# Performance work log

Measured on AMD Instinct MI355X. Metric: run time of the kernel, lower is better.

The kernel has to match this reference:

```python
import jax, jax.numpy as jnp
import numpy as np

E, T, D_H, D_I, R = 8, 4096, 2048, 5632, 128


def setup_inputs() -> dict:
    key = jax.random.key(0)
    ks = jax.random.split(key, 12)
    s = 0.02
    return {
        "x": jax.random.normal(ks[0], (T, D_H), dtype=jnp.float32),
        "expert_idx": jax.random.randint(ks[1], (T,), 0, E),
        # gate: hidden -> intermediate
        "gate_A": jax.random.normal(ks[2], (E, R, D_H), dtype=jnp.float32) * s,
        "gate_C": jax.random.normal(ks[3], (R, R), dtype=jnp.float32) * s,
        "gate_B": jax.random.normal(ks[4], (E, D_I, R), dtype=jnp.float32) * s,
        # up: hidden -> intermediate
        "up_A": jax.random.normal(ks[5], (E, R, D_H), dtype=jnp.float32) * s,
        "up_C": jax.random.normal(ks[6], (R, R), dtype=jnp.float32) * s,
        "up_B": jax.random.normal(ks[7], (E, D_I, R), dtype=jnp.float32) * s,
        # down: intermediate -> hidden, with per-expert bias
        "down_A": jax.random.normal(ks[8], (E, R, D_I), dtype=jnp.float32) * s,
        "down_C": jax.random.normal(ks[9], (R, R), dtype=jnp.float32) * s,
        "down_B": jax.random.normal(ks[10], (E, D_H, R), dtype=jnp.float32) * s,
        "down_bias": jax.random.normal(ks[11], (E, D_H), dtype=jnp.float32) * s,
    }


def _shared_core(x, A, C, B, onehot_et):
    # x: [t, d_in]; A: [e, r, d_in]; C: [r, r]; B: [e, d_out, r]; onehot_et: [e, t]
    # per-token expert weight W_e = B_e @ C @ A_e; mask early so zeros propagate
    h = jnp.einsum('td,erd->etr', x, A) * onehot_et[:, :, None]  # [e, t, r]
    h = jnp.einsum('etr,sr->ets', h, C)                           # [e, t, r]
    return jnp.einsum('ets,eds->td', h, B)                        # [t, d_out]


def reference(x, expert_idx, gate_A, gate_C, gate_B, up_A, up_C, up_B,
              down_A, down_C, down_B, down_bias):
    onehot = jax.nn.one_hot(expert_idx, E, dtype=x.dtype).T  # [E, T]
    g = jax.nn.silu(_shared_core(x, gate_A, gate_C, gate_B, onehot))  # [T, D_I]
    u = _shared_core(x, up_A, up_C, up_B, onehot)                     # [T, D_I]
    down = _shared_core(g * u, down_A, down_C, down_B, onehot)        # [T, D_H]
    return down + down_bias[expert_idx]
```

## Files before the change

### kernel.cpp

```cpp
#include <hip/hip_runtime.h>
#include <hip/hip_bf16.h>

#define E_  8
#define T_  4096
#define DH_ 2048
#define DI_ 5632
#define R_  128
#define TILE_ 64
#define NT_ 72
#define TPMAX_ (NT_*TILE_)

typedef short bf16x8 __attribute__((ext_vector_type(8)));
typedef short bf16x4 __attribute__((ext_vector_type(4)));
typedef float f32x4 __attribute__((ext_vector_type(4)));

#define MFMA(a, b, c) __builtin_amdgcn_mfma_f32_16x16x32_bf16((a), (b), (c), 0, 0, 0)

__device__ __forceinline__ unsigned short f2bf(float f) {
  union { float f; unsigned u; } v; v.f = f;
  return (unsigned short)((v.u + 0x7fffu + ((v.u >> 16) & 1u)) >> 16);
}

__device__ __forceinline__ bf16x8 cvt8(float4 a, float4 b) {
  bf16x8 o;
  o[0] = (short)f2bf(a.x); o[1] = (short)f2bf(a.y);
  o[2] = (short)f2bf(a.z); o[3] = (short)f2bf(a.w);
  o[4] = (short)f2bf(b.x); o[5] = (short)f2bf(b.y);
  o[6] = (short)f2bf(b.z); o[7] = (short)f2bf(b.w);
  return o;
}

__device__ __forceinline__ int tile_expert(int s0, const int* off) {
  int e = 0;
#pragma unroll
  for (int q = 1; q < E_; q++) if (s0 >= off[q]) e = q;
  return e;
}

__global__ __launch_bounds__(1024) void k_route(
    const int* __restrict__ idx, int* __restrict__ off, int* __restrict__ tok)
{
  __shared__ int cnt[E_], cur[E_], offs[E_ + 1];
  const int tid = threadIdx.x;
  if (tid < E_) cnt[tid] = 0;
  __syncthreads();
  for (int t = tid; t < T_; t += 1024) atomicAdd(&cnt[idx[t]], 1);
  __syncthreads();
  if (tid == 0) {
    int a = 0;
    for (int e = 0; e < E_; e++) {
      offs[e] = a; cur[e] = a;
      a += ((cnt[e] + TILE_ - 1) / TILE_) * TILE_;
    }
    offs[E_] = a;
  }
  __syncthreads();
  if (tid <= E_) off[tid] = offs[tid];
  for (int t = tid; t < T_; t += 1024) {
    int p = atomicAdd(&cur[idx[t]], 1);
    tok[p] = t;
  }
}

__global__ __launch_bounds__(256) void k_cvt(
    const float* __restrict__ gA, const float* __restrict__ uA,
    const float* __restrict__ gB, const float* __restrict__ uB,
    const float* __restrict__ dA, const float* __restrict__ dB,
    const float* __restrict__ gC, const float* __restrict__ uC,
    const float* __restrict__ dC,
    short* __restrict__ gAb, short* __restrict__ uAb,
    short* __restrict__ gBb, short* __restrict__ uBb,
    short* __restrict__ dAb, short* __restrict__ dBb,
    short* __restrict__ gCb, short* __restrict__ uCb,
    short* __restrict__ dCb)
{
  long i = (long)(blockIdx.x * 256 + threadIdx.x) * 4;
  const float* s; short* d;
  if      (i <  4194304) { if (i < 2097152) { s = gA; d = gAb; } else { s = uA; d = uAb; i -= 2097152; } }
  else if (i <  9961472) { s = gB; d = gBb; i -= 4194304; }
  else if (i < 15728640) { s = uB; d = uBb; i -= 9961472; }
  else if (i < 21495808) { s = dA; d = dAb; i -= 15728640; }
  else if (i < 23592960) { s = dB; d = dBb; i -= 21495808; }
  else if (i < 23609344) { s = gC; d = gCb; i -= 23592960; }
  else if (i < 23625728) { s = uC; d = uCb; i -= 23609344; }
  else if (i < 23642112) { s = dC; d = dCb; i -= 23625728; }
  else return;
  float4 v = *(const float4*)(s + i);
  bf16x4 o;
  o[0] = (short)f2bf(v.x); o[1] = (short)f2bf(v.y);
  o[2] = (short)f2bf(v.z); o[3] = (short)f2bf(v.w);
  *(bf16x4*)(d + i) = o;
}

__global__ __launch_bounds__(256) void k_gather(
    const float* __restrict__ x, const int* __restrict__ tok,
    short* __restrict__ Xb)
{
  const int p = blockIdx.x;
  const int t = tok[p];
  const int c = threadIdx.x * 8;
  bf16x8 o;
  if (t >= 0) {
    float4 v0 = *(const float4*)(x + (size_t)t * DH_ + c);
    float4 v1 = *(const float4*)(x + (size_t)t * DH_ + c + 4);
    o = cvt8(v0, v1);
  } else {
    o = (bf16x8){0, 0, 0, 0, 0, 0, 0, 0};
  }
  *(bf16x8*)(Xb + (size_t)p * DH_ + c) = o;
}

__global__ __launch_bounds__(256) void k_stage1(
    const short* __restrict__ Xb,
    const short* __restrict__ gAb, const short* __restrict__ uAb,
    const int* __restrict__ off, float* __restrict__ Hp)
{
  const int s0 = blockIdx.x * TILE_;
  if (s0 >= off[E_]) return;
  const int e = tile_expert(s0, off);
  const int y = blockIdx.y, kc = blockIdx.z;
  const short* A = (y ? uAb : gAb) + (size_t)e * R_ * DH_ + kc * 512;

  const int tid = threadIdx.x;
  const int lane = tid & 63, wv = tid >> 6;
  const int col = lane & 15, quad = lane >> 4;

  const short* xb = Xb + (size_t)(s0 + col) * DH_ + kc * 512 + quad * 8;
  const short* ab = A + (size_t)(wv * 32 + col) * DH_ + quad * 8;

  f32x4 acc[4][2] = {};
#pragma unroll 4
  for (int k0 = 0; k0 < 512; k0 += 32) {
    bf16x8 b0 = *(const bf16x8*)(ab + k0);
    bf16x8 b1 = *(const bf16x8*)(ab + (size_t)16 * DH_ + k0);
#pragma unroll
    for (int m = 0; m < 4; m++) {
      bf16x8 a = *(const bf16x8*)(xb + (size_t)m * 16 * DH_ + k0);
      acc[m][0] = MFMA(a, b0, acc[m][0]);
      acc[m][1] = MFMA(a, b1, acc[m][1]);
    }
  }
  float* O = Hp + (size_t)(y * 4 + kc) * TPMAX_ * R_;
#pragma unroll
  for (int m = 0; m < 4; m++)
#pragma unroll
    for (int nl = 0; nl < 2; nl++)
#pragma unroll
      for (int r = 0; r < 4; r++)
        O[(size_t)(s0 + m * 16 + quad * 4 + r) * R_ + (wv * 2 + nl) * 16 + col] =
            acc[m][nl][r];
}

__global__ __launch_bounds__(256) void k_stage1b(
    const float* __restrict__ Hp,
    const short* __restrict__ gCb, const short* __restrict__ uCb,
    const int* __restrict__ off,
    short* __restrict__ Hgb, short* __restrict__ Hub)
{
  const int s0 = blockIdx.x * TILE_;
  if (s0 >= off[E_]) return;
  const int y = blockIdx.y;
  const short* C = y ? uCb : gCb;
  short* H = y ? Hub : Hgb;

  __shared__ short h1s[64][136];
  const int tid = threadIdx.x;
  {
    const int lg = tid >> 2, lq = (tid & 3) * 32;
    const float* base = Hp + ((size_t)y * 4 * TPMAX_ + s0 + lg) * R_ + lq;
    float s[32] = {};
#pragma unroll
    for (int kc = 0; kc < 4; kc++) {
      const float* p = base + (size_t)kc * TPMAX_ * R_;
#pragma unroll
      for (int q = 0; q < 8; q++) {
        float4 v = *(const float4*)(p + q * 4);
        s[q * 4 + 0] += v.x; s[q * 4 + 1] += v.y;
        s[q * 4 + 2] += v.z; s[q * 4 + 3] += v.w;
      }
    }
#pragma unroll
    for (int j = 0; j < 32; j++) h1s[lg][lq + j] = (short)f2bf(s[j]);
  }
  __syncthreads();

  const int lane = tid & 63, wv = tid >> 6;
  const int col = lane & 15, quad = lane >> 4;
  f32x4 acc2[4][2] = {};
#pragma unroll
  for (int kk = 0; kk < 4; kk++) {
    bf16x8 b[2];
#pragma unroll
    for (int nl = 0; nl < 2; nl++)
      b[nl] = *(const bf16x8*)(C + (size_t)((wv * 2 + nl) * 16 + col) * R_ +
                               kk * 32 + quad * 8);
#pragma unroll
    for (int m = 0; m < 4; m++) {
      bf16x8 a = *(const bf16x8*)&h1s[m * 16 + col][kk * 32 + quad * 8];
      acc2[m][0] = MFMA(a, b[0], acc2[m][0]);
      acc2[m][1] = MFMA(a, b[1], acc2[m][1]);
    }
  }
#pragma unroll
  for (int m = 0; m < 4; m++)
#pragma unroll
    for (int nl = 0; nl < 2; nl++)
#pragma unroll
      for (int r = 0; r < 4; r++)
        H[(size_t)(s0 + m * 16 + quad * 4 + r) * R_ + (wv * 2 + nl) * 16 + col] =
            (short)f2bf(acc2[m][nl][r]);
}

__global__ __launch_bounds__(256, 2) void k_stage2(
    const short* __restrict__ Hgb, const short* __restrict__ Hub,
    const short* __restrict__ gBb, const short* __restrict__ uBb,
    const short* __restrict__ dAb,
    const int* __restrict__ off, float* __restrict__ Hd1)
{
  const int e = blockIdx.x;
  const int i0 = blockIdx.y * 128;
  const int lo = off[e], hi = off[e + 1];
  if (lo >= hi) return;
  const short* Bg = gBb + (size_t)e * DI_ * R_;
  const short* Bu = uBb + (size_t)e * DI_ * R_;
  const short* Ad = dAb + (size_t)e * R_ * DI_;

  const int tid = threadIdx.x;
  const int lane = tid & 63, wv = tid >> 6;
  const int col = lane & 15, quad = lane >> 4;

  bf16x8 wg[4][2], wu[4][2], wa[4][2];
#pragma unroll
  for (int kk = 0; kk < 4; kk++)
#pragma unroll
    for (int nl = 0; nl < 2; nl++) {
      size_t bo = (size_t)(i0 + (wv * 2 + nl) * 16 + col) * R_ + kk * 32 + quad * 8;
      wg[kk][nl] = *(const bf16x8*)(Bg + bo);
      wu[kk][nl] = *(const bf16x8*)(Bu + bo);
      wa[kk][nl] = *(const bf16x8*)(Ad + (size_t)((wv * 2 + nl) * 16 + col) * DI_ +
                                    i0 + kk * 32 + quad * 8);
    }

  __shared__ short hgs[64][136];
  __shared__ short hus[64][136];
  __shared__ short ZT[64][136];

  for (int s0 = lo; s0 < hi; s0 += TILE_) {
    {
      const int row = tid >> 2, seg = (tid & 3) * 32;
      const short* pg = Hgb + (size_t)(s0 + row) * R_ + seg;
      const short* pu = Hub + (size_t)(s0 + row) * R_ + seg;
#pragma unroll
      for (int q = 0; q < 4; q++) {
        *(bf16x8*)&hgs[row][seg + q * 8] = *(const bf16x8*)(pg + q * 8);
        *(bf16x8*)&hus[row][seg + q * 8] = *(const bf16x8*)(pu + q * 8);
      }
    }
    __syncthreads();

    f32x4 gacc[4][2] = {}, uacc[4][2] = {};
#pragma unroll
    for (int kk = 0; kk < 4; kk++)
#pragma unroll
      for (int m = 0; m < 4; m++) {
        bf16x8 ag = *(const bf16x8*)&hgs[m * 16 + col][kk * 32 + quad * 8];
        bf16x8 au = *(const bf16x8*)&hus[m * 16 + col][kk * 32 + quad * 8];
#pragma unroll
        for (int nl = 0; nl < 2; nl++) {
          gacc[m][nl] = MFMA(ag, wg[kk][nl], gacc[m][nl]);
          uacc[m][nl] = MFMA(au, wu[kk][nl], uacc[m][nl]);
        }
      }
    __syncthreads();

#pragma unroll
    for (int m = 0; m < 4; m++)
#pragma unroll
      for (int nl = 0; nl < 2; nl++)
#pragma unroll
        for (int r = 0; r < 4; r++) {
          float g = gacc[m][nl][r];
          float z = (g / (1.0f + __expf(-g))) * uacc[m][nl][r];
          ZT[m * 16 + quad * 4 + r][(wv * 2 + nl) * 16 + col] = (short)f2bf(z);
        }
    __syncthreads();

    f32x4 dacc[4][2] = {};
#pragma unroll
    for (int kk2 = 0; kk2 < 4; kk2++)
#pragma unroll
      for (int m = 0; m < 4; m++) {
        bf16x8 za = *(const bf16x8*)&ZT[m * 16 + col][kk2 * 32 + quad * 8];
        dacc[m][0] = MFMA(za, wa[kk2][0], dacc[m][0]);
        dacc[m][1] = MFMA(za, wa[kk2][1], dacc[m][1]);
      }
#pragma unroll
    for (int m = 0; m < 4; m++)
#pragma unroll
      for (int nl = 0; nl < 2; nl++)
#pragma unroll
        for (int r = 0; r < 4; r++)
          atomicAdd(&Hd1[(size_t)(s0 + m * 16 + quad * 4 + r) * R_ +
                         (wv * 2 + nl) * 16 + col],
                    dacc[m][nl][r]);
  }
}

__global__ __launch_bounds__(256) void k_applyCd(
    const float* __restrict__ Hd1, const short* __restrict__ dCb,
    const int* __restrict__ off, short* __restrict__ Hd2b)
{
  const int s0 = blockIdx.x * TILE_;
  if (s0 >= off[E_]) return;
  const int tid = threadIdx.x;
  const int lane = tid & 63, wv = tid >> 6;
  const int col = lane & 15, quad = lane >> 4;

  bf16x8 wc[4][2];
#pragma unroll
  for (int kk = 0; kk < 4; kk++)
#pragma unroll
    for (int nl = 0; nl < 2; nl++)
      wc[kk][nl] = *(const bf16x8*)(dCb + (size_t)((wv * 2 + nl) * 16 + col) * R_ +
                                    kk * 32 + quad * 8);

  f32x4 acc[4][2] = {};
#pragma unroll
  for (int kk = 0; kk < 4; kk++)
#pragma unroll
    for (int m = 0; m < 4; m++) {
      const float* hp = Hd1 + (size_t)(s0 + m * 16 + col) * R_ + kk * 32 + quad * 8;
      float4 v0 = *(const float4*)hp;
      float4 v1 = *(const float4*)(hp + 4);
      bf16x8 a = cvt8(v0, v1);
      acc[m][0] = MFMA(a, wc[kk][0], acc[m][0]);
      acc[m][1] = MFMA(a, wc[kk][1], acc[m][1]);
    }
#pragma unroll
  for (int m = 0; m < 4; m++)
#pragma unroll
    for (int nl = 0; nl < 2; nl++)
#pragma unroll
      for (int r = 0; r < 4; r++)
        Hd2b[(size_t)(s0 + m * 16 + quad * 4 + r) * R_ + (wv * 2 + nl) * 16 + col] =
            (short)f2bf(acc[m][nl][r]);
}

__global__ __launch_bounds__(256, 2) void k_stage3(
    const short* __restrict__ Hd2b, const short* __restrict__ dBb,
    const float* __restrict__ dbias,
    const int* __restrict__ off, const int* __restrict__ tok,
    float* __restrict__ out)
{
  const int e = blockIdx.x;
  const int d0 = blockIdx.y * 128;
  const int lo = off[e], hi = off[e + 1];
  const int tid = threadIdx.x;
  const int lane = tid & 63, wv = tid >> 6;
  const int col = lane & 15, quad = lane >> 4;

  bf16x8 wb[4][2];
#pragma unroll
  for (int kk = 0; kk < 4; kk++)
#pragma unroll
    for (int nl = 0; nl < 2; nl++)
      wb[kk][nl] = *(const bf16x8*)(dBb + (size_t)e * DH_ * R_ +
                                    (size_t)(d0 + (wv * 2 + nl) * 16 + col) * R_ +
                                    kk * 32 + quad * 8);
  float bias[2];
#pragma unroll
  for (int nl = 0; nl < 2; nl++)
    bias[nl] = dbias[(size_t)e * DH_ + d0 + (wv * 2 + nl) * 16 + col];

  for (int s0 = lo + (int)blockIdx.z * TILE_; s0 < hi; s0 += 4 * TILE_) {
    f32x4 acc[4][2] = {};
#pragma unroll
    for (int kk = 0; kk < 4; kk++)
#pragma unroll
      for (int m = 0; m < 4; m++) {
        bf16x8 a = *(const bf16x8*)(Hd2b + (size_t)(s0 + m * 16 + col) * R_ +
                                    kk * 32 + quad * 8);
        acc[m][0] = MFMA(a, wb[kk][0], acc[m][0]);
        acc[m][1] = MFMA(a, wb[kk][1], acc[m][1]);
      }
#pragma unroll
    for (int m = 0; m < 4; m++)
#pragma unroll
      for (int r = 0; r < 4; r++) {
        int t = tok[s0 + m * 16 + quad * 4 + r];
        if (t < 0) continue;
#pragma unroll
        for (int nl = 0; nl < 2; nl++) {
          int d = d0 + (wv * 2 + nl) * 16 + col;
          out[(size_t)t * DH_ + d] = acc[m][nl][r] + bias[nl];
        }
      }
  }
}

extern "C" void kernel_launch(void* const* d_in, const int* in_sizes, int n_in,
                              void* d_out, int out_size, void* d_ws, size_t ws_size,
                              hipStream_t stream)
{
  (void)in_sizes; (void)n_in; (void)out_size; (void)ws_size;
  const float* x     = (const float*)d_in[0];
  const int*   idx   = (const int*)d_in[1];
  const float* gA    = (const float*)d_in[2];
  const float* gC    = (const float*)d_in[3];
  const float* gBw   = (const float*)d_in[4];
  const float* uA    = (const float*)d_in[5];
  const float* uC    = (const float*)d_in[6];
  const float* uBw   = (const float*)d_in[7];
  const float* dA    = (const float*)d_in[8];
  const float* dC    = (const float*)d_in[9];
  const float* dBw   = (const float*)d_in[10];
  const float* dbias = (const float*)d_in[11];
  float* out = (float*)d_out;

  char* ws = (char*)d_ws;
  int* off = (int*)ws;
  int* tok = (int*)(ws + 512);
  float* Hd1 = (float*)(ws + 32768);
  float* Hp  = (float*)(ws + 2392064);
  short* Xb  = (short*)(ws + 21266432);
  short* Hgb = (short*)(ws + 40140800);
  short* Hub = (short*)(ws + 41320448);
  short* Hd2b= (short*)(ws + 42500096);
  short* gAb = (short*)(ws + 43679744);
  short* uAb = (short*)(ws + 47874048);
  short* gBb = (short*)(ws + 52068352);
  short* uBb = (short*)(ws + 63602688);
  short* dAb = (short*)(ws + 75137024);
  short* dBb = (short*)(ws + 86671360);
  short* gCb = (short*)(ws + 90865664);
  short* uCb = (short*)(ws + 90898432);
  short* dCb = (short*)(ws + 90931200);

  hipMemsetAsync(tok, 0xFF, TPMAX_ * sizeof(int), stream);
  hipMemsetAsync(Hd1, 0, (size_t)TPMAX_ * R_ * sizeof(float), stream);

  k_cvt    <<<dim3(23088), 256, 0, stream>>>(gA, uA, gBw, uBw, dA, dBw, gC, uC, dC,
                                             gAb, uAb, gBb, uBb, dAb, dBb, gCb, uCb, dCb);
  k_route  <<<1, 1024, 0, stream>>>(idx, off, tok);
  k_gather <<<dim3(TPMAX_), 256, 0, stream>>>(x, tok, Xb);
  k_stage1 <<<dim3(NT_, 2, 4), 256, 0, stream>>>(Xb, gAb, uAb, off, Hp);
  k_stage1b<<<dim3(NT_, 2), 256, 0, stream>>>(Hp, gCb, uCb, off, Hgb, Hub);
  k_stage2 <<<dim3(E_, 44), 256, 0, stream>>>(Hgb, Hub, gBb, uBb, dAb, off, Hd1);
  k_applyCd<<<dim3(NT_), 256, 0, stream>>>(Hd1, dCb, off, Hd2b);
  k_stage3 <<<dim3(E_, 16, 4), 256, 0, stream>>>(Hd2b, dBb, dbias, off, tok, out);
}
```

Baseline: 349.7 us.

## Restructure MoE pipeline: fuse cvt+gather, drop split-K stage1, retile stage2 by token tile

Merges weight conversion and token gather into one launch. Stage1 now splits the output over the rank dimension instead of splitting K, so each block writes bf16 directly with no fp32 partial buffer and no reduction in stage1b. Stage2 moves from per-expert blocks that loop over all of that expert's tokens to per-token-tile blocks that each cover an eighth of the intermediate dimension, streaming the weights. Stage3 is launched with twice the z-parallelism. The changes trade weight reuse within a block for more parallelism and less intermediate memory traffic, and may reread weights more often from cache.

Measured after the change: 349.9 us. No clear change (+0.1%).

```diff
diff --git a/kernel.cpp b/kernel.cpp
--- a/kernel.cpp
+++ b/kernel.cpp
@@ -62,7 +62,9 @@
   }
 }
 
-__global__ __launch_bounds__(256) void k_cvt(
+__global__ __launch_bounds__(256) void k_cvtgather(
+    const float* __restrict__ x, const int* __restrict__ tok,
+    short* __restrict__ Xb,
     const float* __restrict__ gA, const float* __restrict__ uA,
     const float* __restrict__ gB, const float* __restrict__ uB,
     const float* __restrict__ dA, const float* __restrict__ dB,
@@ -74,7 +76,22 @@
     short* __restrict__ gCb, short* __restrict__ uCb,
     short* __restrict__ dCb)
 {
-  long i = (long)(blockIdx.x * 256 + threadIdx.x) * 4;
+  if (blockIdx.x < TPMAX_) {
+    const int p = blockIdx.x;
+    const int t = tok[p];
+    const int c = threadIdx.x * 8;
+    bf16x8 o;
+    if (t >= 0) {
+      float4 v0 = *(const float4*)(x + (size_t)t * DH_ + c);
+      float4 v1 = *(const float4*)(x + (size_t)t * DH_ + c + 4);
+      o = cvt8(v0, v1);
+    } else {
+      o = (bf16x8){0, 0, 0, 0, 0, 0, 0, 0};
+    }
+    *(bf16x8*)(Xb + (size_t)p * DH_ + c) = o;
+    return;
+  }
+  long i = (long)((blockIdx.x - TPMAX_) * 256 + threadIdx.x) * 4;
   const float* s; short* d;
   if      (i <  4194304) { if (i < 2097152) { s = gA; d = gAb; } else { s = uA; d = uAb; i -= 2097152; } }
   else if (i <  9961472) { s = gB; d = gBb; i -= 4194304; }
@@ -92,67 +109,53 @@
   *(bf16x4*)(d + i) = o;
 }
 
-__global__ __launch_bounds__(256) void k_gather(
-    const float* __restrict__ x, const int* __restrict__ tok,
-    short* __restrict__ Xb)
-{
-  const int p = blockIdx.x;
-  const int t = tok[p];
-  const int c = threadIdx.x * 8;
-  bf16x8 o;
-  if (t >= 0) {
-    float4 v0 = *(const float4*)(x + (size_t)t * DH_ + c);
-    float4 v1 = *(const float4*)(x + (size_t)t * DH_ + c + 4);
-    o = cvt8(v0, v1);
-  } else {
-    o = (bf16x8){0, 0, 0, 0, 0, 0, 0, 0};
-  }
-  *(bf16x8*)(Xb + (size_t)p * DH_ + c) = o;
-}
-
-__global__ __launch_bounds__(256) void k_stage1(
+__global__ __launch_bounds__(256, 2) void k_stage1(
     const short* __restrict__ Xb,
     const short* __restrict__ gAb, const short* __restrict__ uAb,
-    const int* __restrict__ off, float* __restrict__ Hp)
-{
-  const int s0 = blockIdx.x * TILE_;
+    const int* __restrict__ off,
+    short* __restrict__ h1gb, short* __restrict__ h1ub)
+{
+  const int id = blockIdx.x;
+  const int rh = id & 1, y = (id >> 1) & 1, tp = (id >> 2) & 1;
+  const int tl = (id >> 3) * 2 + tp;
+  const int s0 = tl * TILE_;
   if (s0 >= off[E_]) return;
   const int e = tile_expert(s0, off);
-  const int y = blockIdx.y, kc = blockIdx.z;
-  const short* A = (y ? uAb : gAb) + (size_t)e * R_ * DH_ + kc * 512;
+  const short* A = (y ? uAb : gAb) + (size_t)e * R_ * DH_ + (size_t)(rh * 64) * DH_;
+  short* H1 = y ? h1ub : h1gb;
 
   const int tid = threadIdx.x;
   const int lane = tid & 63, wv = tid >> 6;
   const int col = lane & 15, quad = lane >> 4;
 
-  const short* xb = Xb + (size_t)(s0 + col) * DH_ + kc * 512 + quad * 8;
-  const short* ab = A + (size_t)(wv * 32 + col) * DH_ + quad * 8;
-
-  f32x4 acc[4][2] = {};
-#pragma unroll 4
-  for (int k0 = 0; k0 < 512; k0 += 32) {
+  const short* xb = Xb + (size_t)(s0 + col) * DH_ + quad * 8;
+  const short* ab = A + (size_t)(wv * 16 + col) * DH_ + quad * 8;
+
+  f32x4 acc[4] = {};
+  for (int k0 = 0; k0 < DH_; k0 += 64) {
     bf16x8 b0 = *(const bf16x8*)(ab + k0);
-    bf16x8 b1 = *(const bf16x8*)(ab + (size_t)16 * DH_ + k0);
+    bf16x8 b1 = *(const bf16x8*)(ab + k0 + 32);
+    bf16x8 a0[4], a1[4];
 #pragma unroll
     for (int m = 0; m < 4; m++) {
-      bf16x8 a = *(const bf16x8*)(xb + (size_t)m * 16 * DH_ + k0);
-      acc[m][0] = MFMA(a, b0, acc[m][0]);
-      acc[m][1] = MFMA(a, b1, acc[m][1]);
-    }
-  }
-  float* O = Hp + (size_t)(y * 4 + kc) * TPMAX_ * R_;
+      a0[m] = *(const bf16x8*)(xb + (size_t)m * 16 * DH_ + k0);
+      a1[m] = *(const bf16x8*)(xb + (size_t)m * 16 * DH_ + k0 + 32);
+    }
+#pragma unroll
+    for (int m = 0; m < 4; m++) acc[m] = MFMA(a0[m], b0, acc[m]);
+#pragma unroll
+    for (int m = 0; m < 4; m++) acc[m] = MFMA(a1[m], b1, acc[m]);
+  }
 #pragma unroll
   for (int m = 0; m < 4; m++)
 #pragma unroll
-    for (int nl = 0; nl < 2; nl++)
-#pragma unroll
-      for (int r = 0; r < 4; r++)
-        O[(size_t)(s0 + m * 16 + quad * 4 + r) * R_ + (wv * 2 + nl) * 16 + col] =
-            acc[m][nl][r];
-}
-
-__global__ __launch_bounds__(256) void k_stage1b(
-    const float* __restrict__ Hp,
+    for (int r = 0; r < 4; r++)
+      H1[(size_t)(s0 + m * 16 + quad * 4 + r) * R_ + rh * 64 + wv * 16 + col] =
+          (short)f2bf(acc[m][r]);
+}
+
+__global__ __launch_bounds__(256, 2) void k_stage1b(
+    const short* __restrict__ h1gb, const short* __restrict__ h1ub,
     const short* __restrict__ gCb, const short* __restrict__ uCb,
     const int* __restrict__ off,
     short* __restrict__ Hgb, short* __restrict__ Hub)
@@ -160,27 +163,18 @@
   const int s0 = blockIdx.x * TILE_;
   if (s0 >= off[E_]) return;
   const int y = blockIdx.y;
+  const short* h1 = y ? h1ub : h1gb;
   const short* C = y ? uCb : gCb;
   short* H = y ? Hub : Hgb;
 
   __shared__ short h1s[64][136];
   const int tid = threadIdx.x;
   {
-    const int lg = tid >> 2, lq = (tid & 3) * 32;
-    const float* base = Hp + ((size_t)y * 4 * TPMAX_ + s0 + lg) * R_ + lq;
-    float s[32] = {};
-#pragma unroll
-    for (int kc = 0; kc < 4; kc++) {
-      const float* p = base + (size_t)kc * TPMAX_ * R_;
-#pragma unroll
-      for (int q = 0; q < 8; q++) {
-        float4 v = *(const float4*)(p + q * 4);
-        s[q * 4 + 0] += v.x; s[q * 4 + 1] += v.y;
-        s[q * 4 + 2] += v.z; s[q * 4 + 3] += v.w;
-      }
-    }
-#pragma unroll
-    for (int j = 0; j < 32; j++) h1s[lg][lq + j] = (short)f2bf(s[j]);
+    const int row = tid >> 2, seg = (tid & 3) * 32;
+    const short* p = h1 + (size_t)(s0 + row) * R_ + seg;
+#pragma unroll
+    for (int q = 0; q < 4; q++)
+      *(bf16x8*)&h1s[row][seg + q * 8] = *(const bf16x8*)(p + q * 8);
   }
   __syncthreads();
 
@@ -211,99 +205,95 @@
             (short)f2bf(acc2[m][nl][r]);
 }
 
-__global__ __launch_bounds__(256, 2) void k_stage2(
+__global__ __launch_bounds__(256, 3) void k_stage2(
     const short* __restrict__ Hgb, const short* __restrict__ Hub,
     const short* __restrict__ gBb, const short* __restrict__ uBb,
     const short* __restrict__ dAb,
     const int* __restrict__ off, float* __restrict__ Hd1)
 {
-  const int e = blockIdx.x;
-  const int i0 = blockIdx.y * 128;
-  const int lo = off[e], hi = off[e + 1];
-  if (lo >= hi) return;
+  const int id = blockIdx.x;
+  const int c = id & 7, tl = id >> 3;
+  const int s0 = tl * TILE_;
+  if (s0 >= off[E_]) return;
+  const int e = tile_expert(s0, off);
+  const int i0 = c * 704;
   const short* Bg = gBb + (size_t)e * DI_ * R_;
   const short* Bu = uBb + (size_t)e * DI_ * R_;
   const short* Ad = dAb + (size_t)e * R_ * DI_;
 
+  __shared__ short hgs[64][136];
+  __shared__ short hus[64][136];
+  __shared__ short ZT[64][72];
+
   const int tid = threadIdx.x;
   const int lane = tid & 63, wv = tid >> 6;
   const int col = lane & 15, quad = lane >> 4;
 
-  bf16x8 wg[4][2], wu[4][2], wa[4][2];
-#pragma unroll
-  for (int kk = 0; kk < 4; kk++)
-#pragma unroll
-    for (int nl = 0; nl < 2; nl++) {
-      size_t bo = (size_t)(i0 + (wv * 2 + nl) * 16 + col) * R_ + kk * 32 + quad * 8;
-      wg[kk][nl] = *(const bf16x8*)(Bg + bo);
-      wu[kk][nl] = *(const bf16x8*)(Bu + bo);
-      wa[kk][nl] = *(const bf16x8*)(Ad + (size_t)((wv * 2 + nl) * 16 + col) * DI_ +
-                                    i0 + kk * 32 + quad * 8);
-    }
-
-  __shared__ short hgs[64][136];
-  __shared__ short hus[64][136];
-  __shared__ short ZT[64][136];
-
-  for (int s0 = lo; s0 < hi; s0 += TILE_) {
-    {
-      const int row = tid >> 2, seg = (tid & 3) * 32;
-      const short* pg = Hgb + (size_t)(s0 + row) * R_ + seg;
-      const short* pu = Hub + (size_t)(s0 + row) * R_ + seg;
-#pragma unroll
-      for (int q = 0; q < 4; q++) {
-        *(bf16x8*)&hgs[row][seg + q * 8] = *(const bf16x8*)(pg + q * 8);
-        *(bf16x8*)&hus[row][seg + q * 8] = *(const bf16x8*)(pu + q * 8);
-      }
-    }
-    __syncthreads();
-
-    f32x4 gacc[4][2] = {}, uacc[4][2] = {};
-#pragma unroll
-    for (int kk = 0; kk < 4; kk++)
+  {
+    const int row = tid >> 2, seg = (tid & 3) * 32;
+    const short* pg = Hgb + (size_t)(s0 + row) * R_ + seg;
+    const short* pu = Hub + (size_t)(s0 + row) * R_ + seg;
+#pragma unroll
+    for (int q = 0; q < 4; q++) {
+      *(bf16x8*)&hgs[row][seg + q * 8] = *(const bf16x8*)(pg + q * 8);
+      *(bf16x8*)&hus[row][seg + q * 8] = *(const bf16x8*)(pu + q * 8);
+    }
+  }
+  __syncthreads();
+
+  f32x4 dacc[4][2] = {};
+
+  for (int sub = 0; sub < 11; sub++) {
+    const int ib = i0 + sub * 64;
+    const int cg = ib + wv * 16 + col;
+    f32x4 gacc[4] = {}, uacc[4] = {};
+#pragma unroll
+    for (int kk = 0; kk < 4; kk++) {
+      bf16x8 bg = *(const bf16x8*)(Bg + (size_t)cg * R_ + kk * 32 + quad * 8);
+      bf16x8 bu = *(const bf16x8*)(Bu + (size_t)cg * R_ + kk * 32 + quad * 8);
 #pragma unroll
       for (int m = 0; m < 4; m++) {
         bf16x8 ag = *(const bf16x8*)&hgs[m * 16 + col][kk * 32 + quad * 8];
         bf16x8 au = *(const bf16x8*)&hus[m * 16 + col][kk * 32 + quad * 8];
-#pragma unroll
-        for (int nl = 0; nl < 2; nl++) {
-          gacc[m][nl] = MFMA(ag, wg[kk][nl], gacc[m][nl]);
-          uacc[m][nl] = MFMA(au, wu[kk][nl], uacc[m][nl]);
-        }
+        gacc[m] = MFMA(ag, bg, gacc[m]);
+        uacc[m] = MFMA(au, bu, uacc[m]);
+      }
+    }
+    __syncthreads();
+#pragma unroll
+    for (int m = 0; m < 4; m++)
+#pragma unroll
+      for (int r = 0; r < 4; r++) {
+        float g = gacc[m][r];
+        float z = (g / (1.0f + __expf(-g))) * uacc[m][r];
+        ZT[m * 16 + quad * 4 + r][wv * 16 + col] = (short)f2bf(z);
       }
     __syncthreads();
-
-#pragma unroll
-    for (int m = 0; m < 4; m++)
-#pragma unroll
-      for (int nl = 0; nl < 2; nl++)
-#pragma unroll
-        for (int r = 0; r < 4; r++) {
-          float g = gacc[m][nl][r];
-          float z = (g / (1.0f + __expf(-g))) * uacc[m][nl][r];
-          ZT[m * 16 + quad * 4 + r][(wv * 2 + nl) * 16 + col] = (short)f2bf(z);
-        }
-    __syncthreads();
-
-    f32x4 dacc[4][2] = {};
-#pragma unroll
-    for (int kk2 = 0; kk2 < 4; kk2++)
-#pragma unroll
-      for (int m = 0; m < 4; m++) {
-        bf16x8 za = *(const bf16x8*)&ZT[m * 16 + col][kk2 * 32 + quad * 8];
-        dacc[m][0] = MFMA(za, wa[kk2][0], dacc[m][0]);
-        dacc[m][1] = MFMA(za, wa[kk2][1], dacc[m][1]);
+#pragma unroll
+    for (int kk2 = 0; kk2 < 2; kk2++) {
+      bf16x8 za[4];
+#pragma unroll
+      for (int m = 0; m < 4; m++)
+        za[m] = *(const bf16x8*)&ZT[m * 16 + col][kk2 * 32 + quad * 8];
+#pragma unroll
+      for (int nl = 0; nl < 2; nl++) {
+        bf16x8 ba = *(const bf16x8*)(Ad + (size_t)((wv * 2 + nl) * 16 + col) * DI_ +
+                                     ib + kk2 * 32 + quad * 8);
+#pragma unroll
+        for (int m = 0; m < 4; m++)
+          dacc[m][nl] = MFMA(za[m], ba, dacc[m][nl]);
       }
-#pragma unroll
-    for (int m = 0; m < 4; m++)
-#pragma unroll
-      for (int nl = 0; nl < 2; nl++)
-#pragma unroll
-        for (int r = 0; r < 4; r++)
-          atomicAdd(&Hd1[(size_t)(s0 + m * 16 + quad * 4 + r) * R_ +
-                         (wv * 2 + nl) * 16 + col],
-                    dacc[m][nl][r]);
-  }
+    }
+  }
+#pragma unroll
+  for (int m = 0; m < 4; m++)
+#pragma unroll
+    for (int nl = 0; nl < 2; nl++)
+#pragma unroll
+      for (int r = 0; r < 4; r++)
+        atomicAdd(&Hd1[(size_t)(s0 + m * 16 + quad * 4 + r) * R_ +
+                       (wv * 2 + nl) * 16 + col],
+                  dacc[m][nl][r]);
 }
 
 __global__ __launch_bounds__(256) void k_applyCd(
@@ -372,7 +362,7 @@
   for (int nl = 0; nl < 2; nl++)
     bias[nl] = dbias[(size_t)e * DH_ + d0 + (wv * 2 + nl) * 16 + col];
 
-  for (int s0 = lo + (int)blockIdx.z * TILE_; s0 < hi; s0 += 4 * TILE_) {
+  for (int s0 = lo + (int)blockIdx.z * TILE_; s0 < hi; s0 += 8 * TILE_) {
     f32x4 acc[4][2] = {};
 #pragma unroll
     for (int kk = 0; kk < 4; kk++)
@@ -421,31 +411,32 @@
   int* off = (int*)ws;
   int* tok = (int*)(ws + 512);
   float* Hd1 = (float*)(ws + 32768);
-  float* Hp  = (float*)(ws + 2392064);
-  short* Xb  = (short*)(ws + 21266432);
-  short* Hgb = (short*)(ws + 40140800);
-  short* Hub = (short*)(ws + 41320448);
-  short* Hd2b= (short*)(ws + 42500096);
-  short* gAb = (short*)(ws + 43679744);
-  short* uAb = (short*)(ws + 47874048);
-  short* gBb = (short*)(ws + 52068352);
-  short* uBb = (short*)(ws + 63602688);
-  short* dAb = (short*)(ws + 75137024);
-  short* dBb = (short*)(ws + 86671360);
-  short* gCb = (short*)(ws + 90865664);
-  short* uCb = (short*)(ws + 90898432);
-  short* dCb = (short*)(ws + 90931200);
+  short* Xb  = (short*)(ws + 2392064);
+  short* h1gb= (short*)(ws + 21266432);
+  short* h1ub= (short*)(ws + 22446080);
+  short* Hgb = (short*)(ws + 23625728);
+  short* Hub = (short*)(ws + 24805376);
+  short* Hd2b= (short*)(ws + 25985024);
+  short* gAb = (short*)(ws + 27164672);
+  short* uAb = (short*)(ws + 31358976);
+  short* gBb = (short*)(ws + 35553280);
+  short* uBb = (short*)(ws + 47087616);
+  short* dAb = (short*)(ws + 58621952);
+  short* dBb = (short*)(ws + 70156288);
+  short* gCb = (short*)(ws + 74350592);
+  short* uCb = (short*)(ws + 74383360);
+  short* dCb = (short*)(ws + 74416128);
 
   hipMemsetAsync(tok, 0xFF, TPMAX_ * sizeof(int), stream);
   hipMemsetAsync(Hd1, 0, (size_t)TPMAX_ * R_ * sizeof(float), stream);
 
-  k_cvt    <<<dim3(23088), 256, 0, stream>>>(gA, uA, gBw, uBw, dA, dBw, gC, uC, dC,
-                                             gAb, uAb, gBb, uBb, dAb, dBb, gCb, uCb, dCb);
-  k_route  <<<1, 1024, 0, stream>>>(idx, off, tok);
-  k_gather <<<dim3(TPMAX_), 256, 0, stream>>>(x, tok, Xb);
-  k_stage1 <<<dim3(NT_, 2, 4), 256, 0, stream>>>(Xb, gAb, uAb, off, Hp);
-  k_stage1b<<<dim3(NT_, 2), 256, 0, stream>>>(Hp, gCb, uCb, off, Hgb, Hub);
-  k_stage2 <<<dim3(E_, 44), 256, 0, stream>>>(Hgb, Hub, gBb, uBb, dAb, off, Hd1);
-  k_applyCd<<<dim3(NT_), 256, 0, stream>>>(Hd1, dCb, off, Hd2b);
-  k_stage3 <<<dim3(E_, 16, 4), 256, 0, stream>>>(Hd2b, dBb, dbias, off, tok, out);
-}
+  k_route    <<<1, 1024, 0, stream>>>(idx, off, tok);
+  k_cvtgather<<<dim3(TPMAX_ + 23088), 256, 0, stream>>>(
+      x, tok, Xb, gA, uA, gBw, uBw, dA, dBw, gC, uC, dC,
+      gAb, uAb, gBb, uBb, dAb, dBb, gCb, uCb, dCb);
+  k_stage1   <<<dim3(288), 256, 0, stream>>>(Xb, gAb, uAb, off, h1gb, h1ub);
+  k_stage1b  <<<dim3(NT_, 2), 256, 0, stream>>>(h1gb, h1ub, gCb, uCb, off, Hgb, Hub);
+  k_stage2   <<<dim3(8 * NT_), 256, 0, stream>>>(Hgb, Hub, gBb, uBb, dAb, off, Hd1);
+  k_applyCd  <<<dim3(NT_), 256, 0, stream>>>(Hd1, dCb, off, Hd2b);
+  k_stage3   <<<dim3(E_, 16, 8), 256, 0, stream>>>(Hd2b, dBb, dbias, off, tok, out);
+}
```
